# Optimization experiments

Hardware: AMD Instinct MI355X
Metric: run time of the kernel (lower is better)

The kernel has to match this reference:

```python
import jax, jax.numpy as jnp
import numpy as np

N_NODES = 1_000_000
N_EDGES = 32_000_000
N_SPECIES = 100
A0 = 0.5291772105638411
KE = 14.399645351950548


def softplus_inverse(x):
    return x + jnp.log(-jnp.expm1(-x))


def setup_inputs() -> dict:
    key = jax.random.key(0)
    k1, k2, k3, k4, k5 = jax.random.split(key, 5)
    node_species = jax.random.randint(k1, (N_NODES,), 0, N_SPECIES, dtype=jnp.int32)
    distances = jax.random.uniform(k2, (N_EDGES,), dtype=jnp.float32)
    cutoffs = jax.random.uniform(k3, (N_EDGES,), dtype=jnp.float32)
    senders = jax.random.randint(k4, (N_EDGES,), 0, N_NODES, dtype=jnp.int32)
    receivers = jax.random.randint(k5, (N_EDGES,), 0, N_NODES, dtype=jnp.int32)
    index_to_z = jnp.arange(1, N_SPECIES + 1, dtype=jnp.int32)
    # learned params (raw, softplus applied in reference) at their constant inits
    a_raw = softplus_inverse(jnp.array([3.2, 0.9423, 0.4028, 0.2016], dtype=jnp.float32))
    c_raw = softplus_inverse(jnp.array([0.1818, 0.5099, 0.2802, 0.02817], dtype=jnp.float32))
    p_raw = jnp.full((1,), softplus_inverse(jnp.float32(0.23)), dtype=jnp.float32)
    d_raw = jnp.full((1,), softplus_inverse(jnp.float32(1.0 / (0.8854 * A0))), dtype=jnp.float32)
    return {
        'node_species': node_species, 'distances': distances, 'cutoffs': cutoffs,
        'senders': senders, 'receivers': receivers, 'index_to_z': index_to_z,
        'a_raw': a_raw, 'c_raw': c_raw, 'p_raw': p_raw, 'd_raw': d_raw,
    }


def reference(node_species, distances, cutoffs, senders, receivers, index_to_z,
              a_raw, c_raw, p_raw, d_raw):
    a = jax.nn.softplus(a_raw)                       # [4]
    c = jax.nn.softplus(c_raw)
    c = c / jnp.sum(c)                               # [4]
    p = jax.nn.softplus(p_raw)                       # [1]
    d = jax.nn.softplus(d_raw)                       # [1]

    z = index_to_z[node_species]                     # [N]
    z_i = z[receivers].astype(jnp.float32)           # [E]
    z_j = z[senders].astype(jnp.float32)             # [E]

    x = KE * cutoffs * z_i * z_j / (distances + 1e-08)              # [E]
    rzd = distances * (jnp.power(z_i, p) + jnp.power(z_j, p)) * d   # [E]
    y = jnp.sum(c * jnp.exp(-a * rzd[:, None]), axis=-1)            # [E]

    scaled_d = distances / 1.5
    sigma_d = jnp.exp(-1.0 / jnp.where(scaled_d > 1e-08, scaled_d, 1e-08))
    sigma_1_d = jnp.exp(-1.0 / jnp.where(1 - scaled_d > 1e-08, 1 - scaled_d, 1e-08))
    w = sigma_1_d / (sigma_1_d + sigma_d)

    energy_rep = w * x * y / 2                                       # [E]
    return jax.ops.segment_sum(energy_rep, receivers, num_segments=node_species.shape[0])
```

## Files before the change

### kernel.cpp

```cpp
#include <hip/hip_runtime.h>

#define SPECIES_CAP 128
#define WS_A   0
#define WS_C   4
#define WS_ZF  16
#define WS_ZPD (16 + SPECIES_CAP)

#define NB       256
#define RSHIFT   12
#define RNODES   4096
#define NSUB     4
#define CNT_STRIDE 16

#define ITER     16
#define CHUNK    (ITER / 4)
#define TILE     (256 * ITER)

#define PARAMS_OFF 0
#define CNT_OFF    4096
#define CNT_BYTES  ((size_t)NB * NSUB * CNT_STRIDE * 4)
#define PAIRS_OFF  (CNT_OFF + CNT_BYTES)

__global__ void zbl_setup(const float* __restrict__ a_raw,
                          const float* __restrict__ c_raw,
                          const float* __restrict__ p_raw,
                          const float* __restrict__ d_raw,
                          const int* __restrict__ index_to_z,
                          int n_species,
                          float* __restrict__ params)
{
    __shared__ float s_p, s_d;
    int t = threadIdx.x;
    if (t == 0) {
        float a[4], c[4];
        float csum = 0.0f;
        for (int i = 0; i < 4; ++i) {
            a[i] = log1pf(expf(a_raw[i]));
            c[i] = log1pf(expf(c_raw[i]));
            csum += c[i];
        }
        for (int i = 0; i < 4; ++i) {
            params[WS_A + i] = a[i];
            params[WS_C + i] = c[i] / csum;
        }
        float p = log1pf(expf(p_raw[0]));
        float d = log1pf(expf(d_raw[0]));
        params[8] = p;
        params[9] = d;
        s_p = p;
        s_d = d;
    }
    __syncthreads();
    float p = s_p, d = s_d;
    for (int s = t; s < n_species && s < SPECIES_CAP; s += blockDim.x) {
        float z = (float)index_to_z[s];
        params[WS_ZF + s]  = z;
        params[WS_ZPD + s] = powf(z, p) * d;
    }
}

__device__ __forceinline__ float zbl_energy(
    float dist, float cut, int snd, int rcv,
    const int* __restrict__ node_species,
    const float* s_zf, const float* s_zpd,
    const float* s_a, const float* s_c)
{
    int si = node_species[rcv];
    int sj = node_species[snd];
    float zi = s_zf[si];
    float zj = s_zf[sj];
    float x = cut * zi * zj / (dist + 1e-8f);
    float rzd = dist * (s_zpd[si] + s_zpd[sj]);
    float y = s_c[0] * __expf(-s_a[0] * rzd)
            + s_c[1] * __expf(-s_a[1] * rzd)
            + s_c[2] * __expf(-s_a[2] * rzd)
            + s_c[3] * __expf(-s_a[3] * rzd);
    float sd = dist * (1.0f / 1.5f);
    float u1 = (sd > 1e-8f) ? sd : 1e-8f;
    float u2 = ((1.0f - sd) > 1e-8f) ? (1.0f - sd) : 1e-8f;
    float e_d  = __expf(-1.0f / u1);
    float e_1d = __expf(-1.0f / u2);
    float w = e_1d / (e_1d + e_d);
    return 7.199822675975274f * w * x * y;
}

__global__ __launch_bounds__(256) void zbl_bin_kernel(
    const float* __restrict__ distances,
    const float* __restrict__ cutoffs,
    const int* __restrict__ senders,
    const int* __restrict__ receivers,
    const int* __restrict__ node_species,
    const float* __restrict__ params,
    unsigned* __restrict__ cnt,
    uint2* __restrict__ pairs,
    int cap,
    float* __restrict__ out,
    int E)
{
    __shared__ float s_zf[SPECIES_CAP];
    __shared__ float s_zpd[SPECIES_CAP];
    __shared__ float s_a[4];
    __shared__ float s_c[4];
    __shared__ unsigned h_cnt[NB];
    __shared__ unsigned h_lbase[NB];
    __shared__ unsigned h_gbase[NB];
    __shared__ unsigned wtot[4];
    __shared__ unsigned s_total;
    __shared__ uint2 stg[TILE];
    int t = threadIdx.x;
    if (t < 4)              s_a[t]     = params[WS_A + t];
    else if (t < 8)         s_c[t - 4] = params[WS_C + (t - 4)];
    for (int s = t; s < SPECIES_CAP; s += 256) {
        s_zf[s]  = params[WS_ZF + s];
        s_zpd[s] = params[WS_ZPD + s];
    }
    h_cnt[t] = 0u;
    __syncthreads();

    float    en[ITER];
    unsigned pk[ITER];
    unsigned vmask = 0u;
    int sub = blockIdx.x & (NSUB - 1);

#pragma unroll
    for (int c = 0; c < CHUNK; ++c) {
        int vbase = (blockIdx.x * (256 * CHUNK) + c * 256 + t) * 4;
        if (vbase + 4 <= E) {
            float4 d4 = *(const float4*)(distances + vbase);
            float4 c4 = *(const float4*)(cutoffs + vbase);
            int4   s4 = *(const int4*)(senders + vbase);
            int4   r4 = *(const int4*)(receivers + vbase);
            int   sn[4] = { s4.x, s4.y, s4.z, s4.w };
            int   rr[4] = { r4.x, r4.y, r4.z, r4.w };
            float dd[4] = { d4.x, d4.y, d4.z, d4.w };
            float cc[4] = { c4.x, c4.y, c4.z, c4.w };
#pragma unroll
            for (int k = 0; k < 4; ++k)
                en[c * 4 + k] = zbl_energy(dd[k], cc[k], sn[k], rr[k],
                                           node_species, s_zf, s_zpd, s_a, s_c);
#pragma unroll
            for (int k = 0; k < 4; ++k) {
                unsigned b  = ((unsigned)rr[k]) >> RSHIFT;
                unsigned rk = atomicAdd(&h_cnt[b], 1u);
                pk[c * 4 + k] = (rk << 20) | (unsigned)rr[k];
                vmask |= 1u << (c * 4 + k);
            }
        } else {
#pragma unroll
            for (int k = 0; k < 4; ++k) {
                int e = vbase + k;
                if (e < E) {
                    int rcv = receivers[e];
                    en[c * 4 + k] = zbl_energy(distances[e], cutoffs[e],
                                               senders[e], rcv,
                                               node_species, s_zf, s_zpd,
                                               s_a, s_c);
                    unsigned b  = ((unsigned)rcv) >> RSHIFT;
                    unsigned rk = atomicAdd(&h_cnt[b], 1u);
                    pk[c * 4 + k] = (rk << 20) | (unsigned)rcv;
                    vmask |= 1u << (c * 4 + k);
                }
            }
        }
    }
    __syncthreads();

    {
        unsigned orig = h_cnt[t];
        unsigned v = orig;
        int lane = t & 63;
#pragma unroll
        for (int d = 1; d < 64; d <<= 1) {
            unsigned nv = __shfl_up(v, d, 64);
            if (lane >= d) v += nv;
        }
        if (lane == 63) wtot[t >> 6] = v;
        __syncthreads();
        unsigned off = 0;
        int wid = t >> 6;
#pragma unroll
        for (int w = 0; w < 3; ++w)
            if (w < wid) off += wtot[w];
        unsigned incl = off + v;
        h_lbase[t] = incl - orig;
        h_gbase[t] = orig
            ? atomicAdd(&cnt[(t * NSUB + sub) * CNT_STRIDE], orig) : 0u;
        if (t == 255) s_total = incl;
    }
    __syncthreads();

#pragma unroll
    for (int k = 0; k < ITER; ++k) {
        if ((vmask >> k) & 1u) {
            unsigned u   = pk[k];
            unsigned rcv = u & 0xFFFFFu;
            unsigned rk  = u >> 20;
            unsigned b   = rcv >> RSHIFT;
            stg[h_lbase[b] + rk] = make_uint2(rcv, __float_as_uint(en[k]));
        }
    }
    __syncthreads();

    unsigned total = s_total;
    for (unsigned i = t; i < total; i += 256) {
        uint2 q = stg[i];
        unsigned b   = q.x >> RSHIFT;
        unsigned pos = h_gbase[b] + (i - h_lbase[b]);
        if (pos < (unsigned)cap)
            pairs[(size_t)(b * NSUB + sub) * cap + pos] = q;
        else
            unsafeAtomicAdd(out + q.x, __uint_as_float(q.y));
    }
}

__global__ __launch_bounds__(256) void zbl_reduce_kernel(
    const unsigned* __restrict__ cnt,
    const uint2* __restrict__ pairs,
    int cap,
    float* __restrict__ out,
    int n_nodes)
{
    __shared__ float acc[RNODES];
    int bs = blockIdx.x;
    int b  = bs / NSUB;
    int t  = threadIdx.x;
    for (int i = t; i < RNODES; i += 256) acc[i] = 0.0f;
    __syncthreads();

    int entries = min((int)cnt[bs * CNT_STRIDE], cap);
    const uint2* pb  = pairs + (size_t)bs * cap;
    const uint4* pb4 = (const uint4*)pb;
    int n2 = entries >> 1;
    for (int j = t; j < n2; j += 256) {
        uint4 q = pb4[j];
        atomicAdd(&acc[q.x & (RNODES - 1)], __uint_as_float(q.y));
        atomicAdd(&acc[q.z & (RNODES - 1)], __uint_as_float(q.w));
    }
    if ((entries & 1) && t == 0) {
        uint2 pr = pb[entries - 1];
        atomicAdd(&acc[pr.x & (RNODES - 1)], __uint_as_float(pr.y));
    }
    __syncthreads();

    int nbase = b << RSHIFT;
    int nmax  = n_nodes - nbase;
    if (nmax <= 0) return;
    int lim = (nmax < RNODES) ? nmax : RNODES;
    for (int i = t; i < lim; i += 256) {
        float v = acc[i];
        if (v != 0.0f) unsafeAtomicAdd(out + nbase + i, v);
    }
}

__global__ __launch_bounds__(256) void zbl_direct_kernel(
    const float* __restrict__ distances,
    const float* __restrict__ cutoffs,
    const int* __restrict__ senders,
    const int* __restrict__ receivers,
    const int* __restrict__ node_species,
    const float* __restrict__ params,
    float* __restrict__ out,
    int E)
{
    __shared__ float s_zf[SPECIES_CAP];
    __shared__ float s_zpd[SPECIES_CAP];
    __shared__ float s_a[4];
    __shared__ float s_c[4];
    int t = threadIdx.x;
    if (t < 4)              s_a[t]     = params[WS_A + t];
    else if (t < 8)         s_c[t - 4] = params[WS_C + (t - 4)];
    for (int s = t; s < SPECIES_CAP; s += blockDim.x) {
        s_zf[s]  = params[WS_ZF + s];
        s_zpd[s] = params[WS_ZPD + s];
    }
    __syncthreads();
    int base = (blockIdx.x * 256 + t) * 4;
    int lim = min(base + 4, E);
    for (int e = base; e < lim; ++e) {
        int rcv = receivers[e];
        float en = zbl_energy(distances[e], cutoffs[e], senders[e], rcv,
                              node_species, s_zf, s_zpd, s_a, s_c);
        unsafeAtomicAdd(out + rcv, en);
    }
}

extern "C" void kernel_launch(void* const* d_in, const int* in_sizes, int n_in,
                              void* d_out, int out_size, void* d_ws, size_t ws_size,
                              hipStream_t stream)
{
    const int*   node_species = (const int*)d_in[0];
    const float* distances    = (const float*)d_in[1];
    const float* cutoffs      = (const float*)d_in[2];
    const int*   senders      = (const int*)d_in[3];
    const int*   receivers    = (const int*)d_in[4];
    const int*   index_to_z   = (const int*)d_in[5];
    const float* a_raw        = (const float*)d_in[6];
    const float* c_raw        = (const float*)d_in[7];
    const float* p_raw        = (const float*)d_in[8];
    const float* d_raw        = (const float*)d_in[9];

    int E         = in_sizes[1];
    int n_species = in_sizes[5];
    int n_nodes   = in_sizes[0];
    float*    out    = (float*)d_out;
    float*    params = (float*)((char*)d_ws + PARAMS_OFF);
    unsigned* cnt    = (unsigned*)((char*)d_ws + CNT_OFF);
    uint2*    pairs  = (uint2*)((char*)d_ws + PAIRS_OFF);

    size_t avail = (ws_size > PAIRS_OFF) ? (ws_size - PAIRS_OFF) : 0;
    long long cap_ll = (long long)(avail / ((size_t)NB * NSUB * sizeof(uint2)));
    int want = E / (NB * NSUB) + E / (NB * NSUB * 4) + 1024;
    int cap = (int)((cap_ll < (long long)want) ? cap_ll : (long long)want);
    cap &= ~1;

    hipMemsetAsync(d_out, 0, (size_t)out_size * sizeof(float), stream);
    zbl_setup<<<1, 128, 0, stream>>>(a_raw, c_raw, p_raw, d_raw,
                                     index_to_z, n_species, params);

    if (cap >= 4096 && n_nodes <= (1 << 20)) {
        hipMemsetAsync(cnt, 0, CNT_BYTES, stream);
        int blocks = (E + TILE - 1) / TILE;
        zbl_bin_kernel<<<blocks, 256, 0, stream>>>(
            distances, cutoffs, senders, receivers, node_species,
            params, cnt, pairs, cap, out, E);
        zbl_reduce_kernel<<<NB * NSUB, 256, 0, stream>>>(
            cnt, pairs, cap, out, n_nodes);
    } else {
        int blocks = ((E + 3) / 4 + 255) / 256;
        zbl_direct_kernel<<<blocks, 256, 0, stream>>>(
            distances, cutoffs, senders, receivers, node_species,
            params, out, E);
    }
}
```

Baseline: 1.035 ms.

## Pack node species to bytes and batch gathers in larger bin blocks

Adds a pre-pass that narrows node_species from int32 to uint8, so the random per-edge species gathers touch a table a quarter the size and more of it stays in cache. The binning kernel now runs 512-thread blocks with 8 edges per thread. It loads all edge data first, then issues every species gather before doing any math, so more memory requests are in flight at once. Divisions are replaced by hardware reciprocal approximations, which adds a small precision risk and an extra kernel launch; the split barrier in the scan relies on both branches reaching a matching __syncthreads.

```diff
diff --git a/kernel.cpp b/kernel.cpp
--- a/kernel.cpp
+++ b/kernel.cpp
@@ -12,14 +12,14 @@
 #define NSUB     4
 #define CNT_STRIDE 16
 
-#define ITER     16
+#define BTHREADS 512
+#define ITER     8
 #define CHUNK    (ITER / 4)
-#define TILE     (256 * ITER)
+#define TILE     (BTHREADS * ITER)
 
 #define PARAMS_OFF 0
 #define CNT_OFF    4096
 #define CNT_BYTES  ((size_t)NB * NSUB * CNT_STRIDE * 4)
-#define PAIRS_OFF  (CNT_OFF + CNT_BYTES)
 
 __global__ void zbl_setup(const float* __restrict__ a_raw,
                           const float* __restrict__ c_raw,
@@ -59,37 +59,49 @@
     }
 }
 
-__device__ __forceinline__ float zbl_energy(
-    float dist, float cut, int snd, int rcv,
-    const int* __restrict__ node_species,
+__global__ __launch_bounds__(256) void zbl_pack8(
+    const int* __restrict__ ns, unsigned char* __restrict__ sp8, int n)
+{
+    int i4 = (blockIdx.x * 256 + threadIdx.x) * 4;
+    if (i4 + 4 <= n) {
+        int4 v = *(const int4*)(ns + i4);
+        *(uchar4*)(sp8 + i4) = make_uchar4((unsigned char)v.x,
+                                           (unsigned char)v.y,
+                                           (unsigned char)v.z,
+                                           (unsigned char)v.w);
+    } else {
+        for (int j = i4; j < n; ++j) sp8[j] = (unsigned char)ns[j];
+    }
+}
+
+__device__ __forceinline__ float zbl_energy2(
+    float dist, float cut, int si, int sj,
     const float* s_zf, const float* s_zpd,
     const float* s_a, const float* s_c)
 {
-    int si = node_species[rcv];
-    int sj = node_species[snd];
     float zi = s_zf[si];
     float zj = s_zf[sj];
-    float x = cut * zi * zj / (dist + 1e-8f);
+    float x = cut * zi * zj * __builtin_amdgcn_rcpf(dist + 1e-8f);
     float rzd = dist * (s_zpd[si] + s_zpd[sj]);
     float y = s_c[0] * __expf(-s_a[0] * rzd)
             + s_c[1] * __expf(-s_a[1] * rzd)
             + s_c[2] * __expf(-s_a[2] * rzd)
             + s_c[3] * __expf(-s_a[3] * rzd);
     float sd = dist * (1.0f / 1.5f);
-    float u1 = (sd > 1e-8f) ? sd : 1e-8f;
-    float u2 = ((1.0f - sd) > 1e-8f) ? (1.0f - sd) : 1e-8f;
-    float e_d  = __expf(-1.0f / u1);
-    float e_1d = __expf(-1.0f / u2);
-    float w = e_1d / (e_1d + e_d);
+    float u1 = fmaxf(sd, 1e-8f);
+    float u2 = fmaxf(1.0f - sd, 1e-8f);
+    float e_d  = __expf(-__builtin_amdgcn_rcpf(u1));
+    float e_1d = __expf(-__builtin_amdgcn_rcpf(u2));
+    float w = e_1d * __builtin_amdgcn_rcpf(e_1d + e_d);
     return 7.199822675975274f * w * x * y;
 }
 
-__global__ __launch_bounds__(256) void zbl_bin_kernel(
+__global__ __launch_bounds__(512, 6) void zbl_bin_kernel(
     const float* __restrict__ distances,
     const float* __restrict__ cutoffs,
     const int* __restrict__ senders,
     const int* __restrict__ receivers,
-    const int* __restrict__ node_species,
+    const unsigned char* __restrict__ sp8,
     const float* __restrict__ params,
     unsigned* __restrict__ cnt,
     uint2* __restrict__ pairs,
@@ -110,62 +122,74 @@
     int t = threadIdx.x;
     if (t < 4)              s_a[t]     = params[WS_A + t];
     else if (t < 8)         s_c[t - 4] = params[WS_C + (t - 4)];
-    for (int s = t; s < SPECIES_CAP; s += 256) {
+    for (int s = t; s < SPECIES_CAP; s += BTHREADS) {
         s_zf[s]  = params[WS_ZF + s];
         s_zpd[s] = params[WS_ZPD + s];
     }
-    h_cnt[t] = 0u;
+    if (t < NB) h_cnt[t] = 0u;
     __syncthreads();
 
     float    en[ITER];
     unsigned pk[ITER];
     unsigned vmask = 0u;
     int sub = blockIdx.x & (NSUB - 1);
-
-#pragma unroll
-    for (int c = 0; c < CHUNK; ++c) {
-        int vbase = (blockIdx.x * (256 * CHUNK) + c * 256 + t) * 4;
-        if (vbase + 4 <= E) {
+    int ebase = blockIdx.x * TILE;
+
+    if (ebase + TILE <= E) {
+        int   rr[ITER], sn[ITER];
+        float dd[ITER], cc[ITER];
+#pragma unroll
+        for (int c = 0; c < CHUNK; ++c) {
+            int vbase = ebase + (c * BTHREADS + t) * 4;
             float4 d4 = *(const float4*)(distances + vbase);
             float4 c4 = *(const float4*)(cutoffs + vbase);
             int4   s4 = *(const int4*)(senders + vbase);
             int4   r4 = *(const int4*)(receivers + vbase);
-            int   sn[4] = { s4.x, s4.y, s4.z, s4.w };
-            int   rr[4] = { r4.x, r4.y, r4.z, r4.w };
-            float dd[4] = { d4.x, d4.y, d4.z, d4.w };
-            float cc[4] = { c4.x, c4.y, c4.z, c4.w };
-#pragma unroll
-            for (int k = 0; k < 4; ++k)
-                en[c * 4 + k] = zbl_energy(dd[k], cc[k], sn[k], rr[k],
-                                           node_species, s_zf, s_zpd, s_a, s_c);
+            rr[c*4+0] = r4.x; rr[c*4+1] = r4.y; rr[c*4+2] = r4.z; rr[c*4+3] = r4.w;
+            sn[c*4+0] = s4.x; sn[c*4+1] = s4.y; sn[c*4+2] = s4.z; sn[c*4+3] = s4.w;
+            dd[c*4+0] = d4.x; dd[c*4+1] = d4.y; dd[c*4+2] = d4.z; dd[c*4+3] = d4.w;
+            cc[c*4+0] = c4.x; cc[c*4+1] = c4.y; cc[c*4+2] = c4.z; cc[c*4+3] = c4.w;
+        }
+        int spi[ITER], spj[ITER];
+#pragma unroll
+        for (int k = 0; k < ITER; ++k) {
+            spi[k] = sp8[rr[k]];
+            spj[k] = sp8[sn[k]];
+        }
+#pragma unroll
+        for (int k = 0; k < ITER; ++k)
+            en[k] = zbl_energy2(dd[k], cc[k], spi[k], spj[k],
+                                s_zf, s_zpd, s_a, s_c);
+#pragma unroll
+        for (int k = 0; k < ITER; ++k) {
+            unsigned b  = ((unsigned)rr[k]) >> RSHIFT;
+            unsigned rk = atomicAdd(&h_cnt[b], 1u);
+            pk[k] = (rk << 20) | (unsigned)rr[k];
+        }
+        vmask = (1u << ITER) - 1u;
+    } else {
+#pragma unroll
+        for (int c = 0; c < CHUNK; ++c) {
 #pragma unroll
             for (int k = 0; k < 4; ++k) {
-                unsigned b  = ((unsigned)rr[k]) >> RSHIFT;
-                unsigned rk = atomicAdd(&h_cnt[b], 1u);
-                pk[c * 4 + k] = (rk << 20) | (unsigned)rr[k];
-                vmask |= 1u << (c * 4 + k);
-            }
-        } else {
-#pragma unroll
-            for (int k = 0; k < 4; ++k) {
-                int e = vbase + k;
+                int e = ebase + (c * BTHREADS + t) * 4 + k;
                 if (e < E) {
                     int rcv = receivers[e];
-                    en[c * 4 + k] = zbl_energy(distances[e], cutoffs[e],
-                                               senders[e], rcv,
-                                               node_species, s_zf, s_zpd,
-                                               s_a, s_c);
+                    int si = sp8[rcv];
+                    int sj = sp8[senders[e]];
+                    en[c*4+k] = zbl_energy2(distances[e], cutoffs[e], si, sj,
+                                            s_zf, s_zpd, s_a, s_c);
                     unsigned b  = ((unsigned)rcv) >> RSHIFT;
                     unsigned rk = atomicAdd(&h_cnt[b], 1u);
-                    pk[c * 4 + k] = (rk << 20) | (unsigned)rcv;
-                    vmask |= 1u << (c * 4 + k);
+                    pk[c*4+k] = (rk << 20) | (unsigned)rcv;
+                    vmask |= 1u << (c*4+k);
                 }
             }
         }
     }
     __syncthreads();
 
-    {
+    if (t < NB) {
         unsigned orig = h_cnt[t];
         unsigned v = orig;
         int lane = t & 63;
@@ -185,7 +209,9 @@
         h_lbase[t] = incl - orig;
         h_gbase[t] = orig
             ? atomicAdd(&cnt[(t * NSUB + sub) * CNT_STRIDE], orig) : 0u;
-        if (t == 255) s_total = incl;
+        if (t == NB - 1) s_total = incl;
+    } else {
+        __syncthreads();
     }
     __syncthreads();
 
@@ -202,7 +228,7 @@
     __syncthreads();
 
     unsigned total = s_total;
-    for (unsigned i = t; i < total; i += 256) {
+    for (unsigned i = t; i < total; i += BTHREADS) {
         uint2 q = stg[i];
         unsigned b   = q.x >> RSHIFT;
         unsigned pos = h_gbase[b] + (i - h_lbase[b]);
@@ -278,8 +304,9 @@
     int lim = min(base + 4, E);
     for (int e = base; e < lim; ++e) {
         int rcv = receivers[e];
-        float en = zbl_energy(distances[e], cutoffs[e], senders[e], rcv,
-                              node_species, s_zf, s_zpd, s_a, s_c);
+        float en = zbl_energy2(distances[e], cutoffs[e],
+                               node_species[rcv], node_species[senders[e]],
+                               s_zf, s_zpd, s_a, s_c);
         unsafeAtomicAdd(out + rcv, en);
     }
 }
@@ -305,9 +332,14 @@
     float*    out    = (float*)d_out;
     float*    params = (float*)((char*)d_ws + PARAMS_OFF);
     unsigned* cnt    = (unsigned*)((char*)d_ws + CNT_OFF);
-    uint2*    pairs  = (uint2*)((char*)d_ws + PAIRS_OFF);
-
-    size_t avail = (ws_size > PAIRS_OFF) ? (ws_size - PAIRS_OFF) : 0;
+
+    size_t spec8_off   = CNT_OFF + CNT_BYTES;
+    size_t spec8_bytes = ((size_t)n_nodes + 4095) & ~(size_t)4095;
+    size_t pairs_off   = spec8_off + spec8_bytes;
+    unsigned char* sp8 = (unsigned char*)d_ws + spec8_off;
+    uint2* pairs       = (uint2*)((char*)d_ws + pairs_off);
+
+    size_t avail = (ws_size > pairs_off) ? (ws_size - pairs_off) : 0;
     long long cap_ll = (long long)(avail / ((size_t)NB * NSUB * sizeof(uint2)));
     int want = E / (NB * NSUB) + E / (NB * NSUB * 4) + 1024;
     int cap = (int)((cap_ll < (long long)want) ? cap_ll : (long long)want);
@@ -317,11 +349,13 @@
     zbl_setup<<<1, 128, 0, stream>>>(a_raw, c_raw, p_raw, d_raw,
                                      index_to_z, n_species, params);
 
-    if (cap >= 4096 && n_nodes <= (1 << 20)) {
+    if (cap >= 4096 && n_nodes <= (1 << 20) && n_species <= SPECIES_CAP) {
         hipMemsetAsync(cnt, 0, CNT_BYTES, stream);
+        int pblocks = (n_nodes / 4 + 255) / 256 + 1;
+        zbl_pack8<<<pblocks, 256, 0, stream>>>(node_species, sp8, n_nodes);
         int blocks = (E + TILE - 1) / TILE;
-        zbl_bin_kernel<<<blocks, 256, 0, stream>>>(
-            distances, cutoffs, senders, receivers, node_species,
+        zbl_bin_kernel<<<blocks, BTHREADS, 0, stream>>>(
+            distances, cutoffs, senders, receivers, sp8,
             params, cnt, pairs, cap, out, E);
         zbl_reduce_kernel<<<NB * NSUB, 256, 0, stream>>>(
             cnt, pairs, cap, out, n_nodes);
```

Result: faster. 908.7 us (-12.2%).
